# Kernel optimization log

Measured on AMD Instinct MI355X. Metric: run time of the kernel, lower is better.

The kernel has to match this reference:

```python
import jax, jax.numpy as jnp
import numpy as np

B, S, D, K = 2, 4096, 512, 32
EPS = 1e-8


def _cantor_measure(n, levels=24):
    """Devil's staircase (Cantor function) evaluated at i/(n-1)."""
    t = np.arange(n, dtype=np.float64) / max(n - 1, 1)
    c = np.zeros(n)
    r = t.copy()
    done = np.zeros(n, dtype=bool)
    scale = 0.5
    for _ in range(levels):
        r = r * 3.0
        d = np.clip(np.floor(r).astype(np.int64), 0, 2)
        r = r - d
        add = np.where(d == 2, scale, 0.0) + np.where(d == 1, scale, 0.0)
        c = np.where(done, c, c + add)
        done = done | (d == 1)
        scale *= 0.5
    return c


def _build_routes_and_weights(n, k):
    """Cantor-distance k-nearest routing (seq_len, k) and normalized fusion weights."""
    c = _cantor_measure(n)
    dist = np.abs(c[:, None] - c[None, :])  # (S, S), built once on host
    idx = np.argsort(dist, axis=1, kind='stable')[:, :k].astype(np.int32)
    d = np.take_along_axis(dist, idx, axis=1)
    w = np.exp(-d)  # geometric 'weighted' fusion mode
    w = w / (w.sum(axis=1, keepdims=True) + EPS)
    return idx, w.astype(np.float32)


def setup_inputs() -> dict:
    key = jax.random.key(0)
    k1, k2, k3, k4 = jax.random.split(key, 4)
    routes_np, weights_np = _build_routes_and_weights(S, K)
    return {
        'x': jax.random.normal(k1, (B, S, D), dtype=jnp.float32),
        'W_in': jax.random.normal(k2, (D, D), dtype=jnp.float32) * (1.0 / np.sqrt(D)),
        'W_out': jax.random.normal(k3, (D, D), dtype=jnp.float32) * (1.0 / np.sqrt(D)),
        'b_out': jax.random.normal(k4, (D,), dtype=jnp.float32) * 0.02,
        'fusion_weights': jnp.asarray(weights_np),
        'routes': jnp.asarray(routes_np),
    }


def reference(x, W_in, W_out, b_out, fusion_weights, routes):
    # 1. input projection (bias-free), heads are a contiguous split of D so
    #    the shared per-position weights make the per-head fuse equal to a flat fuse
    h = x @ W_in                                  # (B, S, D)
    # 2. gather fusion window per position (irregular Cantor routing)
    g = jnp.take(h, routes, axis=1)               # (B, S, K, D)
    # 3. weighted fusion with normalized staircase-distance weights
    fused = jnp.einsum('bskd,sk->bsd', g, fusion_weights)
    # 4. output projection + residual
    out = fused @ W_out + b_out
    return x + out
```

## Files before the change

### kernel.cpp

```cpp
#include <hip/hip_runtime.h>
#include <hip/hip_bf16.h>
#include <stdint.h>

#define S_LEN  4096
#define D_DIM  512
#define K_R    32
#define M_ROWS 8192

typedef __attribute__((ext_vector_type(8))) short bf16x8;
typedef __attribute__((ext_vector_type(4))) float f32x4;

__device__ __forceinline__ float bf2f(short u) {
  union { unsigned int i; float f; } c;
  c.i = ((unsigned int)(unsigned short)u) << 16;
  return c.f;
}

__device__ __forceinline__ void gload_lds16(const void* g, void* lds) {
  __builtin_amdgcn_global_load_lds(
      (__attribute__((address_space(1))) void*)g,
      (__attribute__((address_space(3))) void*)lds, 16, 0, 0);
}

__device__ __forceinline__ int4 pack8(float4 v0, float4 v1) {
  union { __hip_bfloat16 h[8]; int4 v; } u;
  u.h[0] = __float2bfloat16(v0.x); u.h[1] = __float2bfloat16(v0.y);
  u.h[2] = __float2bfloat16(v0.z); u.h[3] = __float2bfloat16(v0.w);
  u.h[4] = __float2bfloat16(v1.x); u.h[5] = __float2bfloat16(v1.y);
  u.h[6] = __float2bfloat16(v1.z); u.h[7] = __float2bfloat16(v1.w);
  return u.v;
}

__global__ void __launch_bounds__(256) prep_kernel(
    const float* __restrict__ x, __hip_bfloat16* __restrict__ xb,
    const float* __restrict__ Win, __hip_bfloat16* __restrict__ Winb,
    const float* __restrict__ Wout, __hip_bfloat16* __restrict__ WoutTb) {
  __shared__ __hip_bfloat16 Lds[64][66];
  const int tid = threadIdx.x;
  if (blockIdx.x < 2048) {
    const int i = blockIdx.x * 256 + tid;
    const float4* xp = (const float4*)x;
    ((int4*)xb)[i] = pack8(xp[2 * i], xp[2 * i + 1]);
    return;
  }
  if (blockIdx.x < 2112) {
    const int e4 = ((blockIdx.x - 2048) * 256 + tid) * 4;
    const float4* wp = (const float4*)Win;
    int4* op = (int4*)Winb;
#pragma unroll
    for (int h = 0; h < 2; ++h)
      op[e4 / 2 + h] = pack8(wp[e4 + 2 * h], wp[e4 + 2 * h + 1]);
    return;
  }
  const int bx = blockIdx.x - 2112;
  const int tr = (bx >> 3) * 64;
  const int tc = (bx & 7) * 64;
#pragma unroll
  for (int it = 0; it < 4; ++it) {
    const int id = it * 256 + tid;
    const int r = id >> 4, c4 = (id & 15) * 4;
    const float4 v = *(const float4*)&Wout[(size_t)(tr + r) * 512 + tc + c4];
    Lds[r][c4]     = __float2bfloat16(v.x);
    Lds[r][c4 + 1] = __float2bfloat16(v.y);
    Lds[r][c4 + 2] = __float2bfloat16(v.z);
    Lds[r][c4 + 3] = __float2bfloat16(v.w);
  }
  __syncthreads();
#pragma unroll
  for (int it = 0; it < 2; ++it) {
    const int id = it * 256 + tid;
    const int j = id >> 3, i0 = (id & 7) * 8;
    union { __hip_bfloat16 h[8]; int4 v; } u;
#pragma unroll
    for (int r = 0; r < 8; ++r) u.h[r] = Lds[i0 + r][j];
    *(int4*)&WoutTb[(size_t)(tc + j) * 512 + tr + i0] = u.v;
  }
}

#define BM 128
#define BN 64
#define BK 64

__global__ void __launch_bounds__(256) mid_kernel(
    const __hip_bfloat16* __restrict__ xb,
    const float* __restrict__ fw,
    const int* __restrict__ routes,
    __hip_bfloat16* __restrict__ g,
    const __hip_bfloat16* __restrict__ WoutTb,
    const __hip_bfloat16* __restrict__ Winb,
    __hip_bfloat16* __restrict__ WcT) {
  __shared__ __hip_bfloat16 As[BM][BK];
  __shared__ __hip_bfloat16 Bs[BN][BK];
  __shared__ float w_s[4][K_R];
  __shared__ int   r_s[4][K_R];
  const int tid = threadIdx.x;
  const int w = tid >> 6, l = tid & 63;

  if (blockIdx.x >= 32) {
    const int lin = blockIdx.x - 32;
    const int bchunk = (lin & 7) * 256 + (lin >> 3);
    const int row = bchunk * 4 + w;
    const int s = row & (S_LEN - 1);
    const int b = row >> 12;
    if (l < K_R) {
      r_s[w][l] = routes[s * K_R + l];
      w_s[w][l] = fw[s * K_R + l];
    }
    __syncthreads();
    const __hip_bfloat16* xbb = xb + (size_t)b * S_LEN * D_DIM + l * 8;
    float acc[8] = {};
#pragma unroll 8
    for (int k = 0; k < K_R; ++k) {
      const float wk = w_s[w][k];
      const bf16x8 v = *(const bf16x8*)(xbb + (size_t)r_s[w][k] * D_DIM);
#pragma unroll
      for (int j = 0; j < 8; ++j) acc[j] = fmaf(wk, bf2f(v[j]), acc[j]);
    }
    union { __hip_bfloat16 h[8]; int4 v; } u;
#pragma unroll
    for (int j = 0; j < 8; ++j) u.h[j] = __float2bfloat16(acc[j]);
    *(int4*)(g + (size_t)row * D_DIM + l * 8) = u.v;
    return;
  }

  const int id2 = blockIdx.x;
  const int bm0 = (id2 >> 3) * BM;
  const int bn0 = (id2 & 7) * BN;
  const int wr  = (w >> 1) * 64;
  const int wcn = (w & 1) * 32;

  const int rin = l >> 3;
  const int usw = (l & 7) ^ rin;
  const __hip_bfloat16* gA = WoutTb + (size_t)(bm0 + w * 8 + rin) * D_DIM + usw * 8;
  const __hip_bfloat16* gB = Winb   + (size_t)(bn0 + w * 8 + rin) * D_DIM + usw * 8;
  __hip_bfloat16* ldsA = &As[w * 8][0];
  __hip_bfloat16* ldsB = &Bs[w * 8][0];
  const int fr = l & 15, fq = l >> 4;

  f32x4 acc[4][2] = {};
  for (int k0 = 0; k0 < D_DIM; k0 += BK) {
#pragma unroll
    for (int i = 0; i < 4; ++i)
      gload_lds16(gA + (size_t)(i * 32) * D_DIM + k0, ldsA + i * 32 * BK);
#pragma unroll
    for (int j = 0; j < 2; ++j)
      gload_lds16(gB + (size_t)(j * 32) * D_DIM + k0, ldsB + j * 32 * BK);
    __syncthreads();
#pragma unroll
    for (int kk = 0; kk < 2; ++kk) {
      const int u = (kk * 4 + fq) ^ (fr & 7);
      bf16x8 af[4], bfv[2];
#pragma unroll
      for (int m = 0; m < 4; ++m)
        af[m] = *(const bf16x8*)&As[wr + m * 16 + fr][u * 8];
#pragma unroll
      for (int n = 0; n < 2; ++n)
        bfv[n] = *(const bf16x8*)&Bs[wcn + n * 16 + fr][u * 8];
#pragma unroll
      for (int m = 0; m < 4; ++m)
#pragma unroll
        for (int n = 0; n < 2; ++n)
          acc[m][n] = __builtin_amdgcn_mfma_f32_16x16x32_bf16(af[m], bfv[n], acc[m][n], 0, 0, 0);
    }
    __syncthreads();
  }
#pragma unroll
  for (int m = 0; m < 4; ++m)
#pragma unroll
    for (int n = 0; n < 2; ++n)
#pragma unroll
      for (int r = 0; r < 4; ++r) {
        const int grow = bm0 + wr + m * 16 + fq * 4 + r;
        const int gcol = bn0 + wcn + n * 16 + fr;
        WcT[(size_t)grow * D_DIM + gcol] = __float2bfloat16(acc[m][n][r]);
      }
}

__global__ void __launch_bounds__(256) gemm_out_kernel(
    const __hip_bfloat16* __restrict__ A,
    const __hip_bfloat16* __restrict__ BT,
    const float* __restrict__ x,
    const float* __restrict__ b_out,
    float* __restrict__ out) {
  __shared__ __hip_bfloat16 As[2][BM][BK];
  __shared__ __hip_bfloat16 Bs[2][BN][BK];
  const int tid = threadIdx.x;
  const int w = tid >> 6, l = tid & 63;

  const int lin = blockIdx.x;
  const int id2 = (lin & 7) * 64 + (lin >> 3);
  const int bm0 = (id2 >> 3) * BM;
  const int bn0 = (id2 & 7) * BN;

  const int wr  = (w >> 1) * 64;
  const int wcn = (w & 1) * 32;

  const int rin = l >> 3;
  const int usw = (l & 7) ^ rin;
  const __hip_bfloat16* gA = A + (size_t)(bm0 + w * 8 + rin) * D_DIM + usw * 8;
  const __hip_bfloat16* gB = BT + (size_t)(bn0 + w * 8 + rin) * D_DIM + usw * 8;

  const int fr = l & 15, fq = l >> 4;
  f32x4 acc[4][2] = {};

#define STAGE(buf, k0)                                                          \
  {                                                                             \
    _Pragma("unroll")                                                           \
    for (int i = 0; i < 4; ++i)                                                 \
      gload_lds16(gA + (size_t)(i * 32) * D_DIM + (k0),                         \
                  &As[buf][w * 8][0] + i * 32 * BK);                            \
    _Pragma("unroll")                                                           \
    for (int j = 0; j < 2; ++j)                                                 \
      gload_lds16(gB + (size_t)(j * 32) * D_DIM + (k0),                         \
                  &Bs[buf][w * 8][0] + j * 32 * BK);                            \
  }

#define COMPUTE(buf)                                                            \
  {                                                                             \
    _Pragma("unroll")                                                           \
    for (int kk = 0; kk < 2; ++kk) {                                            \
      const int u = (kk * 4 + fq) ^ (fr & 7);                                   \
      bf16x8 af[4], bfv[2];                                                     \
      _Pragma("unroll")                                                         \
      for (int m = 0; m < 4; ++m)                                               \
        af[m] = *(const bf16x8*)&As[buf][wr + m * 16 + fr][u * 8];              \
      _Pragma("unroll")                                                         \
      for (int n = 0; n < 2; ++n)                                               \
        bfv[n] = *(const bf16x8*)&Bs[buf][wcn + n * 16 + fr][u * 8];            \
      _Pragma("unroll")                                                         \
      for (int m = 0; m < 4; ++m)                                               \
        _Pragma("unroll")                                                       \
        for (int n = 0; n < 2; ++n)                                             \
          acc[m][n] = __builtin_amdgcn_mfma_f32_16x16x32_bf16(                  \
              af[m], bfv[n], acc[m][n], 0, 0, 0);                               \
    }                                                                           \
  }

  STAGE(0, 0);
  __syncthreads();
  int cur = 0;
#pragma unroll
  for (int t = 0; t < 7; ++t) {
    STAGE(cur ^ 1, (t + 1) * BK);
    COMPUTE(cur);
    __syncthreads();
    cur ^= 1;
  }
  COMPUTE(cur);
#undef STAGE
#undef COMPUTE

  const float bb0 = b_out[bn0 + wcn + fr];
  const float bb1 = b_out[bn0 + wcn + 16 + fr];
#pragma unroll
  for (int m = 0; m < 4; ++m)
#pragma unroll
    for (int r = 0; r < 4; ++r) {
      const int grow = bm0 + wr + m * 16 + fq * 4 + r;
      const size_t base = (size_t)grow * D_DIM + bn0 + wcn + fr;
      out[base]      = acc[m][0][r] + x[base]      + bb0;
      out[base + 16] = acc[m][1][r] + x[base + 16] + bb1;
    }
}

extern "C" void kernel_launch(void* const* d_in, const int* in_sizes, int n_in,
                              void* d_out, int out_size, void* d_ws, size_t ws_size,
                              hipStream_t stream) {
  const float* x      = (const float*)d_in[0];
  const float* W_in   = (const float*)d_in[1];
  const float* W_out  = (const float*)d_in[2];
  const float* b_out  = (const float*)d_in[3];
  const float* fw     = (const float*)d_in[4];
  const int*   routes = (const int*)d_in[5];
  float* out = (float*)d_out;

  char* ws = (char*)d_ws;
  __hip_bfloat16* Xb     = (__hip_bfloat16*)ws;
  __hip_bfloat16* WcT    = (__hip_bfloat16*)(ws + 8388608);
  __hip_bfloat16* g      = (__hip_bfloat16*)(ws + 8912896);
  __hip_bfloat16* Winb   = (__hip_bfloat16*)(ws + 17301504);
  __hip_bfloat16* WoutTb = (__hip_bfloat16*)(ws + 17825792);

  prep_kernel<<<2176, 256, 0, stream>>>(x, Xb, W_in, Winb, W_out, WoutTb);
  mid_kernel<<<2080, 256, 0, stream>>>(Xb, fw, routes, g, WoutTb, Winb, WcT);
  gemm_out_kernel<<<512, 256, 0, stream>>>(g, WcT, x, b_out, out);
}
```

Baseline: 36.19 us.

## Reorder pipeline: fold weight conversion into Wc GEMM, gather after output GEMM

The combined weight Wc = W_in·W_out is now built directly from fp32 W_in and W_out, transposed and converted to bf16 into LDS inside the small GEMM blocks. This removes the separate Winb/WoutTb conversion pass and its dependency. The pipeline is reordered so the dense GEMM runs on converted x first (Y = x·Wc), and the gather-weighted fusion then runs over Y and adds the residual and bias in one fused epilogue. This removes the fp32 output epilogue from the GEMM, but Y is stored in bf16 before the gather, which changes rounding. The in-loop conversion also gives up the async global-to-LDS loads for that small GEMM.

Result: slower. 50.58 us (+39.8%).

```diff
diff --git a/kernel.cpp b/kernel.cpp
--- a/kernel.cpp
+++ b/kernel.cpp
@@ -31,120 +31,67 @@
   return u.v;
 }
 
-__global__ void __launch_bounds__(256) prep_kernel(
+#define BM 128
+#define BN 64
+#define BK 64
+
+__global__ void __launch_bounds__(256) prep_wc_kernel(
     const float* __restrict__ x, __hip_bfloat16* __restrict__ xb,
-    const float* __restrict__ Win, __hip_bfloat16* __restrict__ Winb,
-    const float* __restrict__ Wout, __hip_bfloat16* __restrict__ WoutTb) {
-  __shared__ __hip_bfloat16 Lds[64][66];
+    const float* __restrict__ Win, const float* __restrict__ Wout,
+    __hip_bfloat16* __restrict__ WcT) {
+  __shared__ __hip_bfloat16 As[BM][BK];
+  __shared__ __hip_bfloat16 Bs[BN][BK];
   const int tid = threadIdx.x;
-  if (blockIdx.x < 2048) {
-    const int i = blockIdx.x * 256 + tid;
+
+  if (blockIdx.x >= 32) {
+    const int i = (blockIdx.x - 32) * 256 + tid;
     const float4* xp = (const float4*)x;
     ((int4*)xb)[i] = pack8(xp[2 * i], xp[2 * i + 1]);
     return;
   }
-  if (blockIdx.x < 2112) {
-    const int e4 = ((blockIdx.x - 2048) * 256 + tid) * 4;
-    const float4* wp = (const float4*)Win;
-    int4* op = (int4*)Winb;
-#pragma unroll
-    for (int h = 0; h < 2; ++h)
-      op[e4 / 2 + h] = pack8(wp[e4 + 2 * h], wp[e4 + 2 * h + 1]);
-    return;
-  }
-  const int bx = blockIdx.x - 2112;
-  const int tr = (bx >> 3) * 64;
-  const int tc = (bx & 7) * 64;
-#pragma unroll
-  for (int it = 0; it < 4; ++it) {
-    const int id = it * 256 + tid;
-    const int r = id >> 4, c4 = (id & 15) * 4;
-    const float4 v = *(const float4*)&Wout[(size_t)(tr + r) * 512 + tc + c4];
-    Lds[r][c4]     = __float2bfloat16(v.x);
-    Lds[r][c4 + 1] = __float2bfloat16(v.y);
-    Lds[r][c4 + 2] = __float2bfloat16(v.z);
-    Lds[r][c4 + 3] = __float2bfloat16(v.w);
-  }
-  __syncthreads();
-#pragma unroll
-  for (int it = 0; it < 2; ++it) {
-    const int id = it * 256 + tid;
-    const int j = id >> 3, i0 = (id & 7) * 8;
-    union { __hip_bfloat16 h[8]; int4 v; } u;
-#pragma unroll
-    for (int r = 0; r < 8; ++r) u.h[r] = Lds[i0 + r][j];
-    *(int4*)&WoutTb[(size_t)(tc + j) * 512 + tr + i0] = u.v;
-  }
-}
-
-#define BM 128
-#define BN 64
-#define BK 64
-
-__global__ void __launch_bounds__(256) mid_kernel(
-    const __hip_bfloat16* __restrict__ xb,
-    const float* __restrict__ fw,
-    const int* __restrict__ routes,
-    __hip_bfloat16* __restrict__ g,
-    const __hip_bfloat16* __restrict__ WoutTb,
-    const __hip_bfloat16* __restrict__ Winb,
-    __hip_bfloat16* __restrict__ WcT) {
-  __shared__ __hip_bfloat16 As[BM][BK];
-  __shared__ __hip_bfloat16 Bs[BN][BK];
-  __shared__ float w_s[4][K_R];
-  __shared__ int   r_s[4][K_R];
-  const int tid = threadIdx.x;
-  const int w = tid >> 6, l = tid & 63;
-
-  if (blockIdx.x >= 32) {
-    const int lin = blockIdx.x - 32;
-    const int bchunk = (lin & 7) * 256 + (lin >> 3);
-    const int row = bchunk * 4 + w;
-    const int s = row & (S_LEN - 1);
-    const int b = row >> 12;
-    if (l < K_R) {
-      r_s[w][l] = routes[s * K_R + l];
-      w_s[w][l] = fw[s * K_R + l];
-    }
-    __syncthreads();
-    const __hip_bfloat16* xbb = xb + (size_t)b * S_LEN * D_DIM + l * 8;
-    float acc[8] = {};
-#pragma unroll 8
-    for (int k = 0; k < K_R; ++k) {
-      const float wk = w_s[w][k];
-      const bf16x8 v = *(const bf16x8*)(xbb + (size_t)r_s[w][k] * D_DIM);
-#pragma unroll
-      for (int j = 0; j < 8; ++j) acc[j] = fmaf(wk, bf2f(v[j]), acc[j]);
-    }
-    union { __hip_bfloat16 h[8]; int4 v; } u;
-#pragma unroll
-    for (int j = 0; j < 8; ++j) u.h[j] = __float2bfloat16(acc[j]);
-    *(int4*)(g + (size_t)row * D_DIM + l * 8) = u.v;
-    return;
-  }
 
   const int id2 = blockIdx.x;
   const int bm0 = (id2 >> 3) * BM;
   const int bn0 = (id2 & 7) * BN;
+  const int w = tid >> 6, l = tid & 63;
   const int wr  = (w >> 1) * 64;
   const int wcn = (w & 1) * 32;
-
-  const int rin = l >> 3;
-  const int usw = (l & 7) ^ rin;
-  const __hip_bfloat16* gA = WoutTb + (size_t)(bm0 + w * 8 + rin) * D_DIM + usw * 8;
-  const __hip_bfloat16* gB = Winb   + (size_t)(bn0 + w * 8 + rin) * D_DIM + usw * 8;
-  __hip_bfloat16* ldsA = &As[w * 8][0];
-  __hip_bfloat16* ldsB = &Bs[w * 8][0];
   const int fr = l & 15, fq = l >> 4;
 
   f32x4 acc[4][2] = {};
   for (int k0 = 0; k0 < D_DIM; k0 += BK) {
-#pragma unroll
-    for (int i = 0; i < 4; ++i)
-      gload_lds16(gA + (size_t)(i * 32) * D_DIM + k0, ldsA + i * 32 * BK);
-#pragma unroll
-    for (int j = 0; j < 2; ++j)
-      gload_lds16(gB + (size_t)(j * 32) * D_DIM + k0, ldsB + j * 32 * BK);
+    __syncthreads();
+#pragma unroll
+    for (int it = 0; it < 4; ++it) {
+      const int task = it * 256 + tid;
+      const int jq = (task & 31) * 4;
+      const int pp = (task >> 5) * 2;
+      const float4 fa = *(const float4*)&Wout[(size_t)(k0 + pp) * 512 + bm0 + jq];
+      const float4 fb = *(const float4*)&Wout[(size_t)(k0 + pp + 1) * 512 + bm0 + jq];
+      const float a_[4] = {fa.x, fa.y, fa.z, fa.w};
+      const float b_[4] = {fb.x, fb.y, fb.z, fb.w};
+#pragma unroll
+      for (int t = 0; t < 4; ++t) {
+        const int j = jq + t;
+        union { __hip_bfloat16 h[2]; unsigned int u32; } pk;
+        pk.h[0] = __float2bfloat16(a_[t]);
+        pk.h[1] = __float2bfloat16(b_[t]);
+        char* dst = (char*)&As[0][0] + j * 128 +
+                    (((pp >> 3) ^ (j & 7)) * 16) + (pp & 7) * 2;
+        *(unsigned int*)dst = pk.u32;
+      }
+    }
+#pragma unroll
+    for (int it = 0; it < 2; ++it) {
+      const int task = it * 256 + tid;
+      const int i = task >> 3;
+      const int u = task & 7;
+      const float4 f0 = *(const float4*)&Win[(size_t)(bn0 + i) * 512 + k0 + u * 8];
+      const float4 f1 = *(const float4*)&Win[(size_t)(bn0 + i) * 512 + k0 + u * 8 + 4];
+      const int4 pk = pack8(f0, f1);
+      char* dst = (char*)&Bs[0][0] + i * 128 + ((u ^ (i & 7)) * 16);
+      *(int4*)dst = pk;
+    }
     __syncthreads();
 #pragma unroll
     for (int kk = 0; kk < 2; ++kk) {
@@ -162,7 +109,6 @@
         for (int n = 0; n < 2; ++n)
           acc[m][n] = __builtin_amdgcn_mfma_f32_16x16x32_bf16(af[m], bfv[n], acc[m][n], 0, 0, 0);
     }
-    __syncthreads();
   }
 #pragma unroll
   for (int m = 0; m < 4; ++m)
@@ -176,12 +122,10 @@
       }
 }
 
-__global__ void __launch_bounds__(256) gemm_out_kernel(
+__global__ void __launch_bounds__(256) gemm_y_kernel(
     const __hip_bfloat16* __restrict__ A,
     const __hip_bfloat16* __restrict__ BT,
-    const float* __restrict__ x,
-    const float* __restrict__ b_out,
-    float* __restrict__ out) {
+    __hip_bfloat16* __restrict__ Y) {
   __shared__ __hip_bfloat16 As[2][BM][BK];
   __shared__ __hip_bfloat16 Bs[2][BN][BK];
   const int tid = threadIdx.x;
@@ -250,17 +194,60 @@
 #undef STAGE
 #undef COMPUTE
 
-  const float bb0 = b_out[bn0 + wcn + fr];
-  const float bb1 = b_out[bn0 + wcn + 16 + fr];
 #pragma unroll
   for (int m = 0; m < 4; ++m)
 #pragma unroll
-    for (int r = 0; r < 4; ++r) {
-      const int grow = bm0 + wr + m * 16 + fq * 4 + r;
-      const size_t base = (size_t)grow * D_DIM + bn0 + wcn + fr;
-      out[base]      = acc[m][0][r] + x[base]      + bb0;
-      out[base + 16] = acc[m][1][r] + x[base + 16] + bb1;
-    }
+    for (int n = 0; n < 2; ++n)
+#pragma unroll
+      for (int r = 0; r < 4; ++r) {
+        const int grow = bm0 + wr + m * 16 + fq * 4 + r;
+        const int gcol = bn0 + wcn + n * 16 + fr;
+        Y[(size_t)grow * D_DIM + gcol] = __float2bfloat16(acc[m][n][r]);
+      }
+}
+
+__global__ void __launch_bounds__(256) gather_out_kernel(
+    const __hip_bfloat16* __restrict__ Y,
+    const float* __restrict__ x,
+    const float* __restrict__ b_out,
+    const float* __restrict__ fw,
+    const int* __restrict__ routes,
+    float* __restrict__ out) {
+  __shared__ float w_s[4][K_R];
+  __shared__ int   r_s[4][K_R];
+  const int tid = threadIdx.x;
+  const int w = tid >> 6, l = tid & 63;
+  const int lin = blockIdx.x;
+  const int bchunk = (lin & 7) * 256 + (lin >> 3);
+  const int row = bchunk * 4 + w;
+  const int s = row & (S_LEN - 1);
+  const int b = row >> 12;
+  if (l < K_R) {
+    r_s[w][l] = routes[s * K_R + l];
+    w_s[w][l] = fw[s * K_R + l];
+  }
+  __syncthreads();
+  const __hip_bfloat16* yb = Y + (size_t)b * S_LEN * D_DIM + l * 8;
+  float acc[8] = {};
+#pragma unroll 8
+  for (int k = 0; k < K_R; ++k) {
+    const float wk = w_s[w][k];
+    const bf16x8 v = *(const bf16x8*)(yb + (size_t)r_s[w][k] * D_DIM);
+#pragma unroll
+    for (int j = 0; j < 8; ++j) acc[j] = fmaf(wk, bf2f(v[j]), acc[j]);
+  }
+  const size_t base = (size_t)row * D_DIM + l * 8;
+  const float4 x0 = *(const float4*)&x[base];
+  const float4 x1 = *(const float4*)&x[base + 4];
+  const float4 b0 = *(const float4*)&b_out[l * 8];
+  const float4 b1 = *(const float4*)&b_out[l * 8 + 4];
+  float4 o0, o1;
+  o0.x = x0.x + b0.x + acc[0]; o0.y = x0.y + b0.y + acc[1];
+  o0.z = x0.z + b0.z + acc[2]; o0.w = x0.w + b0.w + acc[3];
+  o1.x = x1.x + b1.x + acc[4]; o1.y = x1.y + b1.y + acc[5];
+  o1.z = x1.z + b1.z + acc[6]; o1.w = x1.w + b1.w + acc[7];
+  *(float4*)&out[base]     = o0;
+  *(float4*)&out[base + 4] = o1;
 }
 
 extern "C" void kernel_launch(void* const* d_in, const int* in_sizes, int n_in,
@@ -275,13 +262,11 @@
   float* out = (float*)d_out;
 
   char* ws = (char*)d_ws;
-  __hip_bfloat16* Xb     = (__hip_bfloat16*)ws;
-  __hip_bfloat16* WcT    = (__hip_bfloat16*)(ws + 8388608);
-  __hip_bfloat16* g      = (__hip_bfloat16*)(ws + 8912896);
-  __hip_bfloat16* Winb   = (__hip_bfloat16*)(ws + 17301504);
-  __hip_bfloat16* WoutTb = (__hip_bfloat16*)(ws + 17825792);
-
-  prep_kernel<<<2176, 256, 0, stream>>>(x, Xb, W_in, Winb, W_out, WoutTb);
-  mid_kernel<<<2080, 256, 0, stream>>>(Xb, fw, routes, g, WoutTb, Winb, WcT);
-  gemm_out_kernel<<<512, 256, 0, stream>>>(g, WcT, x, b_out, out);
-}
+  __hip_bfloat16* Xb  = (__hip_bfloat16*)ws;
+  __hip_bfloat16* WcT = (__hip_bfloat16*)(ws + 8388608);
+  __hip_bfloat16* Y   = (__hip_bfloat16*)(ws + 8912896);
+
+  prep_wc_kernel<<<2080, 256, 0, stream>>>(x, Xb, W_in, W_out, WcT);
+  gemm_y_kernel<<<512, 256, 0, stream>>>(Xb, WcT, Y);
+  gather_out_kernel<<<2048, 256, 0, stream>>>(Y, x, b_out, fw, routes, out);
+}
```

## Reorder pipeline: GEMM with fused weight first, then gather plus residual epilogue

Applied to the files above, without the earlier changes.

Moves the gather-fusion step after the combined projection GEMM (Y = Xb @ Wc), so the gather kernel reads bf16 Y and writes fp32 output with bias and residual directly. The weight-combine GEMM becomes a separate 32-block kernel launched before the main GEMM, which adds a fourth launch and serialises it ahead of the main GEMM. The output GEMM now writes bf16 Y instead of fp32 out, and the vectorised gather epilogue replaces the scattered fp32 stores. The gather no longer overlaps the small Wc GEMM as it did in the shared kernel.

Result: slower. 44.95 us (+24.2%).

```diff
diff --git a/kernel.cpp b/kernel.cpp
--- a/kernel.cpp
+++ b/kernel.cpp
@@ -30,6 +30,10 @@
   u.h[6] = __float2bfloat16(v1.z); u.h[7] = __float2bfloat16(v1.w);
   return u.v;
 }
+
+#define BM 128
+#define BN 64
+#define BK 64
 
 __global__ void __launch_bounds__(256) prep_kernel(
     const float* __restrict__ x, __hip_bfloat16* __restrict__ xb,
@@ -77,51 +81,14 @@
   }
 }
 
-#define BM 128
-#define BN 64
-#define BK 64
-
-__global__ void __launch_bounds__(256) mid_kernel(
-    const __hip_bfloat16* __restrict__ xb,
-    const float* __restrict__ fw,
-    const int* __restrict__ routes,
-    __hip_bfloat16* __restrict__ g,
+__global__ void __launch_bounds__(256) wc_kernel(
     const __hip_bfloat16* __restrict__ WoutTb,
     const __hip_bfloat16* __restrict__ Winb,
     __hip_bfloat16* __restrict__ WcT) {
   __shared__ __hip_bfloat16 As[BM][BK];
   __shared__ __hip_bfloat16 Bs[BN][BK];
-  __shared__ float w_s[4][K_R];
-  __shared__ int   r_s[4][K_R];
   const int tid = threadIdx.x;
   const int w = tid >> 6, l = tid & 63;
-
-  if (blockIdx.x >= 32) {
-    const int lin = blockIdx.x - 32;
-    const int bchunk = (lin & 7) * 256 + (lin >> 3);
-    const int row = bchunk * 4 + w;
-    const int s = row & (S_LEN - 1);
-    const int b = row >> 12;
-    if (l < K_R) {
-      r_s[w][l] = routes[s * K_R + l];
-      w_s[w][l] = fw[s * K_R + l];
-    }
-    __syncthreads();
-    const __hip_bfloat16* xbb = xb + (size_t)b * S_LEN * D_DIM + l * 8;
-    float acc[8] = {};
-#pragma unroll 8
-    for (int k = 0; k < K_R; ++k) {
-      const float wk = w_s[w][k];
-      const bf16x8 v = *(const bf16x8*)(xbb + (size_t)r_s[w][k] * D_DIM);
-#pragma unroll
-      for (int j = 0; j < 8; ++j) acc[j] = fmaf(wk, bf2f(v[j]), acc[j]);
-    }
-    union { __hip_bfloat16 h[8]; int4 v; } u;
-#pragma unroll
-    for (int j = 0; j < 8; ++j) u.h[j] = __float2bfloat16(acc[j]);
-    *(int4*)(g + (size_t)row * D_DIM + l * 8) = u.v;
-    return;
-  }
 
   const int id2 = blockIdx.x;
   const int bm0 = (id2 >> 3) * BM;
@@ -176,12 +143,10 @@
       }
 }
 
-__global__ void __launch_bounds__(256) gemm_out_kernel(
+__global__ void __launch_bounds__(256) gemm_y_kernel(
     const __hip_bfloat16* __restrict__ A,
     const __hip_bfloat16* __restrict__ BT,
-    const float* __restrict__ x,
-    const float* __restrict__ b_out,
-    float* __restrict__ out) {
+    __hip_bfloat16* __restrict__ Y) {
   __shared__ __hip_bfloat16 As[2][BM][BK];
   __shared__ __hip_bfloat16 Bs[2][BN][BK];
   const int tid = threadIdx.x;
@@ -250,17 +215,60 @@
 #undef STAGE
 #undef COMPUTE
 
-  const float bb0 = b_out[bn0 + wcn + fr];
-  const float bb1 = b_out[bn0 + wcn + 16 + fr];
 #pragma unroll
   for (int m = 0; m < 4; ++m)
 #pragma unroll
-    for (int r = 0; r < 4; ++r) {
-      const int grow = bm0 + wr + m * 16 + fq * 4 + r;
-      const size_t base = (size_t)grow * D_DIM + bn0 + wcn + fr;
-      out[base]      = acc[m][0][r] + x[base]      + bb0;
-      out[base + 16] = acc[m][1][r] + x[base + 16] + bb1;
-    }
+    for (int n = 0; n < 2; ++n)
+#pragma unroll
+      for (int r = 0; r < 4; ++r) {
+        const int grow = bm0 + wr + m * 16 + fq * 4 + r;
+        const int gcol = bn0 + wcn + n * 16 + fr;
+        Y[(size_t)grow * D_DIM + gcol] = __float2bfloat16(acc[m][n][r]);
+      }
+}
+
+__global__ void __launch_bounds__(256) gather_out_kernel(
+    const __hip_bfloat16* __restrict__ Y,
+    const float* __restrict__ x,
+    const float* __restrict__ b_out,
+    const float* __restrict__ fw,
+    const int* __restrict__ routes,
+    float* __restrict__ out) {
+  __shared__ float w_s[4][K_R];
+  __shared__ int   r_s[4][K_R];
+  const int tid = threadIdx.x;
+  const int w = tid >> 6, l = tid & 63;
+  const int lin = blockIdx.x;
+  const int bchunk = (lin & 7) * 256 + (lin >> 3);
+  const int row = bchunk * 4 + w;
+  const int s = row & (S_LEN - 1);
+  const int b = row >> 12;
+  if (l < K_R) {
+    r_s[w][l] = routes[s * K_R + l];
+    w_s[w][l] = fw[s * K_R + l];
+  }
+  __syncthreads();
+  const __hip_bfloat16* yb = Y + (size_t)b * S_LEN * D_DIM + l * 8;
+  float acc[8] = {};
+#pragma unroll 8
+  for (int k = 0; k < K_R; ++k) {
+    const float wk = w_s[w][k];
+    const bf16x8 v = *(const bf16x8*)(yb + (size_t)r_s[w][k] * D_DIM);
+#pragma unroll
+    for (int j = 0; j < 8; ++j) acc[j] = fmaf(wk, bf2f(v[j]), acc[j]);
+  }
+  const size_t base = (size_t)row * D_DIM + l * 8;
+  const float4 x0 = *(const float4*)&x[base];
+  const float4 x1 = *(const float4*)&x[base + 4];
+  const float4 b0 = *(const float4*)&b_out[l * 8];
+  const float4 b1 = *(const float4*)&b_out[l * 8 + 4];
+  float4 o0, o1;
+  o0.x = x0.x + b0.x + acc[0]; o0.y = x0.y + b0.y + acc[1];
+  o0.z = x0.z + b0.z + acc[2]; o0.w = x0.w + b0.w + acc[3];
+  o1.x = x1.x + b1.x + acc[4]; o1.y = x1.y + b1.y + acc[5];
+  o1.z = x1.z + b1.z + acc[6]; o1.w = x1.w + b1.w + acc[7];
+  *(float4*)&out[base]     = o0;
+  *(float4*)&out[base + 4] = o1;
 }
 
 extern "C" void kernel_launch(void* const* d_in, const int* in_sizes, int n_in,
@@ -277,11 +285,12 @@
   char* ws = (char*)d_ws;
   __hip_bfloat16* Xb     = (__hip_bfloat16*)ws;
   __hip_bfloat16* WcT    = (__hip_bfloat16*)(ws + 8388608);
-  __hip_bfloat16* g      = (__hip_bfloat16*)(ws + 8912896);
+  __hip_bfloat16* Y      = (__hip_bfloat16*)(ws + 8912896);
   __hip_bfloat16* Winb   = (__hip_bfloat16*)(ws + 17301504);
   __hip_bfloat16* WoutTb = (__hip_bfloat16*)(ws + 17825792);
 
   prep_kernel<<<2176, 256, 0, stream>>>(x, Xb, W_in, Winb, W_out, WoutTb);
-  mid_kernel<<<2080, 256, 0, stream>>>(Xb, fw, routes, g, WoutTb, Winb, WcT);
-  gemm_out_kernel<<<512, 256, 0, stream>>>(g, WcT, x, b_out, out);
-}
+  wc_kernel<<<32, 256, 0, stream>>>(WoutTb, Winb, WcT);
+  gemm_y_kernel<<<512, 256, 0, stream>>>(Xb, WcT, Y);
+  gather_out_kernel<<<2048, 256, 0, stream>>>(Y, x, b_out, fw, routes, out);
+}
```
